# Performance work log

Measured on AMD Instinct MI355X. Metric: run time of the kernel, lower is better.

The kernel has to match this reference:

```python
import jax, jax.numpy as jnp
import numpy as np

K = 25        # moving_avg_window
PAD = (K - 1) // 2
EPS = 1e-8


def _decompose(x):
    # x: [B, S, C]
    B, S, C = x.shape
    # --- trend: AvgPool1d(kernel=K, stride=1, padding=PAD), count_include_pad=True
    # zero-pad then windowed sum, always divide by K (matches torch default).
    sums = jax.lax.reduce_window(
        x, jnp.float32(0.0).astype(x.dtype), jax.lax.add,
        window_dimensions=(1, K, 1), window_strides=(1, 1, 1),
        padding=((0, 0), (PAD, PAD), (0, 0)))
    trend = sums / K  # [B, S, C]

    # --- initial seasonal: FFT along time, zero out first half of bins
    # (including DC), take real part of inverse FFT.
    half = S // 2
    freq_mask = (jnp.arange(S) >= half)[None, :, None]  # [1, S, 1]
    dft = jnp.fft.fft(x, axis=1)
    seasonal0 = jnp.fft.ifft(dft * freq_mask, axis=1).real.astype(x.dtype)

    # --- degrees of trend/seasonality per (batch, channel)
    # Reference uses the robust fallback residual = x - trend - seasonal0
    # (the STL path in the original is a per-series scipy call; its fallback
    # defines the same math).
    resid = x - trend - seasonal0
    var = lambda v: jnp.var(v, axis=1, ddof=1)  # torch.var is unbiased -> ddof=1; [B, C]
    var_res = var(resid)
    d_t = jnp.clip(1.0 - var_res / (var(trend + resid) + EPS), 0.0, 1.0)
    d_s = jnp.clip(1.0 - var_res / (var(seasonal0 + resid) + EPS), 0.0, 1.0)

    # --- final seasonal: multiplicative if strong trend/seasonality, else additive
    cond = ((d_t > 0.5) | (d_s > 0.5))[:, None, :]  # [B, 1, C]
    seasonal = jnp.where(cond, x / (trend + EPS), x - trend)
    return trend, seasonal


def setup_inputs() -> dict:
    key = jax.random.key(0)
    x = jax.random.normal(key, (32, 4096, 128), dtype=jnp.float32)
    return {"x": x}


def reference(x):
    return _decompose(x)
```

## Files before the change

kernel.cpp:

```cpp
#include <hip/hip_runtime.h>

#define SS 4096
#define CC 128
#define BB 32
#define KW 25
#define PADW 12
#define CH 64
#define SROWS (CH + KW - 1)
#define CPB 8
#define NSERIES (BB * CC)
#define STAGE_F4 (SROWS * CC / 4)

typedef float f4v __attribute__((ext_vector_type(4)));
typedef float f2v __attribute__((ext_vector_type(2)));

__global__ __launch_bounds__(512)
void kb_pass(const float* __restrict__ x, float* __restrict__ trend,
             float* __restrict__ seasonal, float* __restrict__ stats) {
    __shared__ f4v stage[2][STAGE_F4];
    __shared__ f2v sred[7][7][64];

    const int blk = blockIdx.x;
    const int b = blk >> 3;
    const int q = blk & 7;
    const int tid = threadIdx.x;
    const int cp = tid & 63;
    const int rg = tid >> 6;
    const float* __restrict__ xb = x + (size_t)b * SS * CC;
    f2v* __restrict__ tb = (f2v*)(trend + (size_t)b * SS * CC);
    f2v* __restrict__ sv = (f2v*)(seasonal + (size_t)b * SS * CC);

    f4v vals[6];
    auto issue = [&](int c) {
        const int sbase = q * (CPB * CH) + c * CH - PADW;
        #pragma unroll
        for (int t = 0; t < 6; ++t) {
            const int idx = t * 512 + tid;
            if (idx < STAGE_F4) {
                const int srow = sbase + (idx >> 5);
                const int crow = srow < 0 ? 0 : (srow >= SS ? SS - 1 : srow);
                vals[t] = *(const f4v*)(xb + (size_t)crow * CC + ((idx & 31) << 2));
            }
        }
    };
    auto commit = [&](int c, int buf) {
        const int sbase = q * (CPB * CH) + c * CH - PADW;
        #pragma unroll
        for (int t = 0; t < 6; ++t) {
            const int idx = t * 512 + tid;
            if (idx < STAGE_F4) {
                f4v w = vals[t];
                const int srow = sbase + (idx >> 5);
                if (srow < 0 || srow >= SS) w = (f4v){0.f, 0.f, 0.f, 0.f};
                stage[buf][idx] = w;
            }
        }
    };

    issue(0);
    commit(0, 0);

    f2v Sx_e = {0,0}, Sx_o = {0,0}, Sx2 = {0,0};
    f2v St_e = {0,0}, St_o = {0,0}, St2 = {0,0}, Sxt = {0,0};

    for (int c = 0; c < CPB; ++c) {
        __syncthreads();
        const int cur = c & 1;
        if (c + 1 < CPB) issue(c + 1);

        const int S0 = q * (CPB * CH) + c * CH;
        const int r0 = rg * 8;
        const f2v* stg = (const f2v*)stage[cur];

        f2v win[KW];
        #pragma unroll
        for (int j = 0; j < KW; ++j) win[j] = stg[(r0 + j) * 64 + cp];

        #pragma unroll
        for (int i = 0; i < 8; ++i) {
            float ax = win[0].x, ay = win[0].y;
            #pragma unroll
            for (int j = 1; j < KW; ++j) { ax += win[j].x; ay += win[j].y; }
            f2v tf;
            tf.x = ax / 25.0f;
            tf.y = ay / 25.0f;
            const int row = (S0 + r0 + i) * 64 + cp;
            __builtin_nontemporal_store(tf, &tb[row]);

            const f2v xv = win[PADW];
            f2v so;
            so.x = xv.x / (tf.x + 1e-8f);
            so.y = xv.y / (tf.y + 1e-8f);
            __builtin_nontemporal_store(so, &sv[row]);

            if (i & 1) { Sx_o.x += xv.x; Sx_o.y += xv.y; St_o.x += tf.x; St_o.y += tf.y; }
            else       { Sx_e.x += xv.x; Sx_e.y += xv.y; St_e.x += tf.x; St_e.y += tf.y; }
            Sx2.x += xv.x * xv.x;  Sx2.y += xv.y * xv.y;
            St2.x += tf.x * tf.x;  St2.y += tf.y * tf.y;
            Sxt.x += xv.x * tf.x;  Sxt.y += xv.y * tf.y;

            #pragma unroll
            for (int j = 0; j < KW - 1; ++j) win[j] = win[j + 1];
            if (i < 7) win[KW - 1] = stg[(r0 + i + KW) * 64 + cp];
        }

        if (c + 1 < CPB) commit(c + 1, cur ^ 1);
    }

    if (rg > 0) {
        f2v* me = &sred[rg - 1][0][cp];
        me[0*64] = Sx_e; me[1*64] = Sx_o; me[2*64] = Sx2;
        me[3*64] = St_e; me[4*64] = St_o; me[5*64] = St2;
        me[6*64] = Sxt;
    }
    __syncthreads();
    if (rg == 0) {
        #pragma unroll
        for (int g = 0; g < 7; ++g) {
            const f2v* gp = &sred[g][0][cp];
            Sx_e.x += gp[0*64].x; Sx_e.y += gp[0*64].y;
            Sx_o.x += gp[1*64].x; Sx_o.y += gp[1*64].y;
            Sx2.x  += gp[2*64].x; Sx2.y  += gp[2*64].y;
            St_e.x += gp[3*64].x; St_e.y += gp[3*64].y;
            St_o.x += gp[4*64].x; St_o.y += gp[4*64].y;
            St2.x  += gp[5*64].x; St2.y  += gp[5*64].y;
            Sxt.x  += gp[6*64].x; Sxt.y  += gp[6*64].y;
        }
        const int series = b * CC + 2 * cp;
        float* sp = stats + (size_t)q * NSERIES + series;
        const size_t jstride = (size_t)CPB * NSERIES;
        *(f2v*)(sp + 0 * jstride) = Sx_e;
        *(f2v*)(sp + 1 * jstride) = Sx_o;
        *(f2v*)(sp + 2 * jstride) = Sx2;
        *(f2v*)(sp + 3 * jstride) = St_e;
        *(f2v*)(sp + 4 * jstride) = St_o;
        *(f2v*)(sp + 5 * jstride) = St2;
        *(f2v*)(sp + 6 * jstride) = Sxt;
    }
}

__global__ __launch_bounds__(256)
void k2_finalize(const float* __restrict__ stats, float* __restrict__ condf) {
    const int j = threadIdx.x >> 5;
    const int sl = threadIdx.x & 31;
    const int series = blockIdx.x * 32 + sl;
    const size_t jstride = (size_t)CPB * NSERIES;

    __shared__ float red[32][8];
    if (j < 7) {
        const float* p = stats + j * jstride + series;
        float a = 0.f;
        #pragma unroll
        for (int k = 0; k < CPB; ++k) a += p[(size_t)k * NSERIES];
        red[sl][j] = a;
    }
    __syncthreads();
    if (threadIdx.x < 32) {
        const int me = threadIdx.x;
        const float Sx_e = red[me][0], Sx_o = red[me][1], Sx2 = red[me][2];
        const float St_e = red[me][3], St_o = red[me][4], St2 = red[me][5];
        const float Sxt = red[me][6];

        const float Sf = (float)SS;
        const float halfS = 0.5f * Sf;
        const float c_e = Sx_o / Sf;
        const float c_o = Sx_e / Sf;
        const float sum_c = halfS * (c_e + c_o);
        const float sumsq_c = halfS * (c_e * c_e + c_o * c_o);

        const float Sw_e = 0.5f * Sx_e - St_e;
        const float Sw_o = 0.5f * Sx_o - St_o;
        const float Sw2 = 0.25f * Sx2 - Sxt + St2;

        const float s1 = (Sw_e + Sw_o) + sum_c;
        const float q1 = Sw2 + 2.f * (c_e * Sw_e + c_o * Sw_o) + sumsq_c;
        const float var1 = (q1 - s1 * s1 / Sf) / (Sf - 1.f);
        const float s2 = 0.5f * (Sx_e + Sx_o) + sum_c;
        const float q2 = 0.25f * Sx2 + (c_e * Sx_e + c_o * Sx_o) + sumsq_c;
        const float var2 = (q2 - s2 * s2 / Sf) / (Sf - 1.f);
        const float Sa = (Sx_e + Sx_o) - (St_e + St_o);
        const float Sa2 = Sx2 - 2.f * Sxt + St2;
        const float var3 = (Sa2 - Sa * Sa / Sf) / (Sf - 1.f);

        const float d_t = 1.f - var1 / (var2 + 1e-8f);
        const float d_s = 1.f - var1 / (var3 + 1e-8f);
        condf[blockIdx.x * 32 + me] = (d_t > 0.5f || d_s > 0.5f) ? 1.f : 0.f;
    }
}

__global__ __launch_bounds__(256)
void k3_fixup(const float* __restrict__ x, const float* __restrict__ trend,
              const float* __restrict__ condf, float* __restrict__ seasonal) {
    const int b = blockIdx.x >> 4;
    const int strip = blockIdx.x & 15;
    const int ch = threadIdx.x & 127;
    const float cnd = condf[b * CC + ch];

    __shared__ int nfalse;
    if (threadIdx.x == 0) nfalse = 0;
    __syncthreads();
    if (threadIdx.x < 128 && cnd <= 0.5f) atomicAdd(&nfalse, 1);
    __syncthreads();
    if (nfalse == 0) return;

    if (cnd <= 0.5f) {
        const int half = threadIdx.x >> 7;
        for (int k = 0; k < 128; ++k) {
            const int s = strip * 256 + 2 * k + half;
            const size_t e = ((size_t)b * SS + s) * CC + ch;
            seasonal[e] = x[e] - trend[e];
        }
    }
}

extern "C" void kernel_launch(void* const* d_in, const int* in_sizes, int n_in,
                              void* d_out, int out_size, void* d_ws, size_t ws_size,
                              hipStream_t stream) {
    const float* x = (const float*)d_in[0];
    float* out = (float*)d_out;
    float* trend = out;
    float* seasonal = out + (size_t)BB * SS * CC;

    float* condf = (float*)d_ws;
    float* stats = condf + NSERIES;

    kb_pass<<<dim3(BB * 8), dim3(512), 0, stream>>>(x, trend, seasonal, stats);
    k2_finalize<<<dim3(NSERIES / 32), dim3(256), 0, stream>>>(stats, condf);
    k3_fixup<<<dim3(BB * 16), dim3(256), 0, stream>>>(x, trend, condf, seasonal);
}
```

Before: 41.20 us.

## Reuse halo rows across chunks and merge finalize with additive fixup kernel

The staging loop now copies the 24 overlapping halo rows between the shared buffers for each new chunk instead of reloading them from global memory. Only the 64 new rows are fetched per chunk, which cuts redundant global reads. The finalize and fixup kernels are merged into one: each block computes the condition for 32 series and rewrites seasonal only for the series that need the additive form. This drops one launch and the condf round trip, at the cost of an extra shared-to-shared copy and strided per-series fixup writes.

```diff
diff --git a/kernel.cpp b/kernel.cpp
--- a/kernel.cpp
+++ b/kernel.cpp
@@ -30,35 +30,59 @@
     f2v* __restrict__ tb = (f2v*)(trend + (size_t)b * SS * CC);
     f2v* __restrict__ sv = (f2v*)(seasonal + (size_t)b * SS * CC);
 
-    f4v vals[6];
-    auto issue = [&](int c) {
-        const int sbase = q * (CPB * CH) + c * CH - PADW;
+    {
+        const int sbase = q * (CPB * CH) - PADW;
+        f4v v0[6];
         #pragma unroll
         for (int t = 0; t < 6; ++t) {
             const int idx = t * 512 + tid;
             if (idx < STAGE_F4) {
                 const int srow = sbase + (idx >> 5);
                 const int crow = srow < 0 ? 0 : (srow >= SS ? SS - 1 : srow);
-                vals[t] = *(const f4v*)(xb + (size_t)crow * CC + ((idx & 31) << 2));
+                v0[t] = *(const f4v*)(xb + (size_t)crow * CC + ((idx & 31) << 2));
             }
         }
-    };
-    auto commit = [&](int c, int buf) {
-        const int sbase = q * (CPB * CH) + c * CH - PADW;
         #pragma unroll
         for (int t = 0; t < 6; ++t) {
             const int idx = t * 512 + tid;
             if (idx < STAGE_F4) {
-                f4v w = vals[t];
+                f4v w = v0[t];
                 const int srow = sbase + (idx >> 5);
                 if (srow < 0 || srow >= SS) w = (f4v){0.f, 0.f, 0.f, 0.f};
-                stage[buf][idx] = w;
+                stage[0][idx] = w;
             }
         }
+    }
+
+    f4v vals[4];
+    auto issue = [&](int c) {
+        const int sbase = q * (CPB * CH) + c * CH - PADW;
+        #pragma unroll
+        for (int t = 0; t < 4; ++t) {
+            const int nidx = t * 512 + tid;
+            const int srow = sbase + 24 + (nidx >> 5);
+            const int crow = srow >= SS ? SS - 1 : srow;
+            vals[t] = *(const f4v*)(xb + (size_t)crow * CC + ((nidx & 31) << 2));
+        }
     };
-
-    issue(0);
-    commit(0, 0);
+    auto commit = [&](int c, int buf) {
+        const f2v* src = (const f2v*)stage[buf ^ 1];
+        f2v* dst = (f2v*)stage[buf];
+        #pragma unroll
+        for (int t = 0; t < 3; ++t) {
+            const int hidx = t * 512 + tid;
+            dst[hidx] = src[64 * 64 + hidx];
+        }
+        const int sbase = q * (CPB * CH) + c * CH - PADW;
+        #pragma unroll
+        for (int t = 0; t < 4; ++t) {
+            const int nidx = t * 512 + tid;
+            const int srow = sbase + 24 + (nidx >> 5);
+            f4v w = vals[t];
+            if (srow >= SS) w = (f4v){0.f, 0.f, 0.f, 0.f};
+            stage[buf][768 + nidx] = w;
+        }
+    };
 
     f2v Sx_e = {0,0}, Sx_o = {0,0}, Sx2 = {0,0};
     f2v St_e = {0,0}, St_o = {0,0}, St2 = {0,0}, Sxt = {0,0};
@@ -140,15 +164,19 @@
 }
 
 __global__ __launch_bounds__(256)
-void k2_finalize(const float* __restrict__ stats, float* __restrict__ condf) {
+void k2_finalize_fix(const float* __restrict__ stats, const float* __restrict__ x,
+                     const float* __restrict__ trend, float* __restrict__ seasonal) {
     const int j = threadIdx.x >> 5;
     const int sl = threadIdx.x & 31;
-    const int series = blockIdx.x * 32 + sl;
+    const int series0 = blockIdx.x * 32;
     const size_t jstride = (size_t)CPB * NSERIES;
 
     __shared__ float red[32][8];
+    __shared__ int nf;
+    __shared__ int flist[32];
+    if (threadIdx.x == 0) nf = 0;
     if (j < 7) {
-        const float* p = stats + j * jstride + series;
+        const float* p = stats + j * jstride + series0 + sl;
         float a = 0.f;
         #pragma unroll
         for (int k = 0; k < CPB; ++k) a += p[(size_t)k * NSERIES];
@@ -184,32 +212,20 @@
 
         const float d_t = 1.f - var1 / (var2 + 1e-8f);
         const float d_s = 1.f - var1 / (var3 + 1e-8f);
-        condf[blockIdx.x * 32 + me] = (d_t > 0.5f || d_s > 0.5f) ? 1.f : 0.f;
-    }
-}
-
-__global__ __launch_bounds__(256)
-void k3_fixup(const float* __restrict__ x, const float* __restrict__ trend,
-              const float* __restrict__ condf, float* __restrict__ seasonal) {
-    const int b = blockIdx.x >> 4;
-    const int strip = blockIdx.x & 15;
-    const int ch = threadIdx.x & 127;
-    const float cnd = condf[b * CC + ch];
-
-    __shared__ int nfalse;
-    if (threadIdx.x == 0) nfalse = 0;
+        if (!(d_t > 0.5f || d_s > 0.5f)) {
+            const int i = atomicAdd(&nf, 1);
+            flist[i] = series0 + me;
+        }
+    }
     __syncthreads();
-    if (threadIdx.x < 128 && cnd <= 0.5f) atomicAdd(&nfalse, 1);
-    __syncthreads();
-    if (nfalse == 0) return;
-
-    if (cnd <= 0.5f) {
-        const int half = threadIdx.x >> 7;
-        for (int k = 0; k < 128; ++k) {
-            const int s = strip * 256 + 2 * k + half;
-            const size_t e = ((size_t)b * SS + s) * CC + ch;
-            seasonal[e] = x[e] - trend[e];
-        }
+    for (int fi = 0; fi < nf; ++fi) {
+        const int sr = flist[fi];
+        const int b = sr >> 7, ch = sr & 127;
+        const float* xs = x + (size_t)b * SS * CC + ch;
+        const float* ts = trend + (size_t)b * SS * CC + ch;
+        float* so = seasonal + (size_t)b * SS * CC + ch;
+        for (int s = threadIdx.x; s < SS; s += 256)
+            so[(size_t)s * CC] = xs[(size_t)s * CC] - ts[(size_t)s * CC];
     }
 }
 
@@ -221,10 +237,8 @@
     float* trend = out;
     float* seasonal = out + (size_t)BB * SS * CC;
 
-    float* condf = (float*)d_ws;
-    float* stats = condf + NSERIES;
+    float* stats = (float*)d_ws;
 
     kb_pass<<<dim3(BB * 8), dim3(512), 0, stream>>>(x, trend, seasonal, stats);
-    k2_finalize<<<dim3(NSERIES / 32), dim3(256), 0, stream>>>(stats, condf);
-    k3_fixup<<<dim3(BB * 16), dim3(256), 0, stream>>>(x, trend, condf, seasonal);
+    k2_finalize_fix<<<dim3(NSERIES / 32), dim3(256), 0, stream>>>(stats, x, trend, seasonal);
 }
```

New measurement: 40.64 us. No clear change (-1.4%).
